# Optimization experiments

Hardware: AMD Instinct MI355X
Metric: run time of the kernel (lower is better)

The kernel has to match this reference:

```python
import jax, jax.numpy as jnp
import numpy as np

D = 1024; NHEAD = 8; NQ = 256; B = 8; HM = 64; WM = 64; S = HM * WM; FF = 4 * D
EPS_LN = 1e-5


def _ln(x, g, b):
    m = x.mean(-1, keepdims=True)
    v = ((x - m) ** 2).mean(-1, keepdims=True)
    return (x - m) / jnp.sqrt(v + EPS_LN) * g + b


def _self_attn(x, w_in, b_in, w_out, b_out, nhead):
    # x: [L, B, D] (torch MultiheadAttention, batch_first=False, eval mode)
    L, Bn, Dm = x.shape
    hd = Dm // nhead
    qkv = x @ w_in.T + b_in  # [L, B, 3D]
    q, k, v = jnp.split(qkv, 3, axis=-1)
    sp = lambda t: t.reshape(L, Bn, nhead, hd).transpose(1, 2, 0, 3)  # [B, H, L, hd]
    q, k, v = sp(q), sp(k), sp(v)
    attn = jax.nn.softmax(jnp.einsum('bhqd,bhkd->bhqk', q, k) / float(hd) ** 0.5, axis=-1)
    out = jnp.einsum('bhqk,bhkd->bhqd', attn, v)
    out = out.transpose(2, 0, 1, 3).reshape(L, Bn, Dm)
    return out @ w_out.T + b_out


def setup_inputs() -> dict:
    key = jax.random.key(0)
    ks = iter(jax.random.split(key, 40))
    nrm = lambda shape: jax.random.normal(next(ks), shape, jnp.float32) * 0.02
    return dict(
        query=jax.random.normal(next(ks), (NQ, B, D), jnp.float32),
        memory=jax.random.normal(next(ks), (S, B, D), jnp.float32),
        prev_mask=jax.random.uniform(next(ks), (B, NQ, HM, WM), dtype=jnp.float32),
        h_mem=HM, w_mem=WM,
        sa_in_w=nrm((3 * D, D)), sa_in_b=jnp.zeros((3 * D,), jnp.float32),
        sa_out_w=nrm((D, D)), sa_out_b=jnp.zeros((D,), jnp.float32),
        ln1_g=jnp.ones((D,), jnp.float32), ln1_b=jnp.zeros((D,), jnp.float32),
        ln2_g=jnp.ones((D,), jnp.float32), ln2_b=jnp.zeros((D,), jnp.float32),
        ln3_g=jnp.ones((D,), jnp.float32), ln3_b=jnp.zeros((D,), jnp.float32),
        wq=nrm((D, D)), bq=jnp.zeros((D,), jnp.float32),
        wk=nrm((D, D)), bk=jnp.zeros((D,), jnp.float32),
        wv=nrm((D, D)), bv=jnp.zeros((D,), jnp.float32),
        wo=nrm((D, D)), bo=jnp.zeros((D,), jnp.float32),
        w1=nrm((FF, D)), b1=jnp.zeros((FF,), jnp.float32),
        w2=nrm((D, FF)), b2=jnp.zeros((D,), jnp.float32),
        mask_w=nrm((S, D)), mask_b=jnp.zeros((S,), jnp.float32),
    )


def reference(query, memory, prev_mask, h_mem, w_mem,
              sa_in_w, sa_in_b, sa_out_w, sa_out_b,
              ln1_g, ln1_b, ln2_g, ln2_b, ln3_g, ln3_b,
              wq, bq, wk, bk, wv, bv, wo, bo,
              w1, b1, w2, b2, mask_w, mask_b):
    nq, Bn, d_model = query.shape
    # --- self attention block ---
    q_norm = _ln(query, ln1_g, ln1_b)
    q2 = _self_attn(q_norm, sa_in_w, sa_in_b, sa_out_w, sa_out_b, NHEAD)
    query = query + q2
    # --- masked cross attention (single-head, as in source) ---
    Q = (_ln(query, ln2_g, ln2_b) @ wq.T + bq).transpose(1, 0, 2)  # [B, NQ, D]
    K = (memory @ wk.T + bk).transpose(1, 0, 2)                    # [B, S, D]
    V = (memory @ wv.T + bv).transpose(1, 0, 2)                    # [B, S, D]
    scores = jnp.einsum('bqd,bsd->bqs', Q, K) / float(d_model) ** 0.5
    scores = scores + jnp.log(prev_mask.reshape(Bn, nq, -1) + 1e-6)
    attn = jax.nn.softmax(scores, axis=-1)
    attn_out = jnp.einsum('bqs,bsd->bqd', attn, V).transpose(1, 0, 2)  # [NQ, B, D]
    query = query + (attn_out @ wo.T + bo)
    # --- FFN ---
    h = jax.nn.gelu(_ln(query, ln3_g, ln3_b) @ w1.T + b1, approximate=False)
    query = query + (h @ w2.T + b2)
    # --- mask prediction ---
    q_for_mask = query.transpose(1, 0, 2)                # [B, NQ, D]
    mask_logits = q_for_mask @ mask_w.T + mask_b          # [B, NQ, H*W]
    pred_mask = jax.nn.sigmoid(mask_logits.reshape(Bn, nq, h_mem, w_mem))
    return (query, pred_mask)
```

## Files before the change

### kernel.cpp

```cpp
#include <hip/hip_runtime.h>
#include <cstdint>


typedef __attribute__((ext_vector_type(8))) __bf16 bf16x8;
typedef __attribute__((ext_vector_type(4))) float f32x4;
typedef __attribute__((ext_vector_type(8))) unsigned short ushort8;
typedef __attribute__((ext_vector_type(4))) unsigned short ushort4v;

__device__ __forceinline__ unsigned short f2bf(float f) {
  return __builtin_bit_cast(unsigned short, (__bf16)f);
}

__global__ __launch_bounds__(256) void cast_bf16_kernel(const float* __restrict__ in,
                                                        unsigned short* __restrict__ out,
                                                        int n8) {
  int i = blockIdx.x * 256 + threadIdx.x;
  if (i >= n8) return;
  const float4* p = (const float4*)in + (size_t)i * 2;
  float4 a = p[0], b = p[1];
  ushort8 o;
  o[0] = f2bf(a.x); o[1] = f2bf(a.y); o[2] = f2bf(a.z); o[3] = f2bf(a.w);
  o[4] = f2bf(b.x); o[5] = f2bf(b.y); o[6] = f2bf(b.z); o[7] = f2bf(b.w);
  ((ushort8*)out)[i] = o;
}

struct CastSegs {
  const float* src[9];
  int cum[10];
};
__global__ __launch_bounds__(256) void cast_multi_kernel(CastSegs cs,
                                                         unsigned short* __restrict__ out) {
  int i = blockIdx.x * 256 + threadIdx.x;
  if (i >= cs.cum[9]) return;
  int s = 0;
  while (i >= cs.cum[s + 1]) s++;
  const float4* p = (const float4*)cs.src[s] + (size_t)(i - cs.cum[s]) * 2;
  float4 a = p[0], b = p[1];
  ushort8 o;
  o[0] = f2bf(a.x); o[1] = f2bf(a.y); o[2] = f2bf(a.z); o[3] = f2bf(a.w);
  o[4] = f2bf(b.x); o[5] = f2bf(b.y); o[6] = f2bf(b.z); o[7] = f2bf(b.w);
  ((ushort8*)out)[i] = o;
}

__global__ __launch_bounds__(256) void bias_concat_kernel(const float* __restrict__ a,
                                                          const float* __restrict__ b,
                                                          float* __restrict__ o) {
  int i = blockIdx.x * 256 + threadIdx.x;
  o[i] = i < 1024 ? a[i] : b[i - 1024];
}

__global__ __launch_bounds__(256) void ln_bf16_kernel(const float* __restrict__ x,
                                                      const float* __restrict__ g,
                                                      const float* __restrict__ b,
                                                      unsigned short* __restrict__ out) {
  int row = blockIdx.x, tid = threadIdx.x;
  const float4* xr = (const float4*)(x + (size_t)row * 1024);
  float4 v = xr[tid];
  float s = v.x + v.y + v.z + v.w;
  float sq = v.x * v.x + v.y * v.y + v.z * v.z + v.w * v.w;
#pragma unroll
  for (int o = 32; o > 0; o >>= 1) { s += __shfl_xor(s, o); sq += __shfl_xor(sq, o); }
  __shared__ float red[8];
  int wave = tid >> 6, lane = tid & 63;
  if (lane == 0) { red[wave] = s; red[4 + wave] = sq; }
  __syncthreads();
  float ts = red[0] + red[1] + red[2] + red[3];
  float tq = red[4] + red[5] + red[6] + red[7];
  float mean = ts * (1.f / 1024.f);
  float var = tq * (1.f / 1024.f) - mean * mean;
  float rstd = rsqrtf(var + 1e-5f);
  float4 gv = ((const float4*)g)[tid];
  float4 bv = ((const float4*)b)[tid];
  ushort4v o;
  o[0] = f2bf((v.x - mean) * rstd * gv.x + bv.x);
  o[1] = f2bf((v.y - mean) * rstd * gv.y + bv.y);
  o[2] = f2bf((v.z - mean) * rstd * gv.z + bv.z);
  o[3] = f2bf((v.w - mean) * rstd * gv.w + bv.w);
  ((ushort4v*)(out + (size_t)row * 1024))[tid] = o;
}

template <bool MASK, int CNT>
__global__ __launch_bounds__(256) void softmax_bf16_kernel(const float* __restrict__ sc,
                                                           const float* __restrict__ pm,
                                                           unsigned short* __restrict__ out,
                                                           float scale) {
  const int L = CNT * 256;
  int row = blockIdx.x, tid = threadIdx.x;
  const float* sr = sc + (size_t)row * L;
  float vals[CNT];
  float mx = -1e30f;
#pragma unroll
  for (int i = 0; i < CNT; i++) {
    int idx = tid + (i << 8);
    float v = sr[idx] * scale;
    if (MASK) v += __logf(pm[(size_t)row * L + idx] + 1e-6f);
    vals[i] = v;
    mx = fmaxf(mx, v);
  }
#pragma unroll
  for (int o = 32; o > 0; o >>= 1) mx = fmaxf(mx, __shfl_xor(mx, o));
  __shared__ float red[8];
  int wave = tid >> 6, lane = tid & 63;
  if (lane == 0) red[wave] = mx;
  __syncthreads();
  mx = fmaxf(fmaxf(red[0], red[1]), fmaxf(red[2], red[3]));
  float sum = 0.f;
#pragma unroll
  for (int i = 0; i < CNT; i++) { vals[i] = __expf(vals[i] - mx); sum += vals[i]; }
#pragma unroll
  for (int o = 32; o > 0; o >>= 1) sum += __shfl_xor(sum, o);
  if (lane == 0) red[4 + wave] = sum;
  __syncthreads();
  float rs = 1.f / (red[4] + red[5] + red[6] + red[7]);
#pragma unroll
  for (int i = 0; i < CNT; i++)
    out[(size_t)row * L + tid + (i << 8)] = f2bf(vals[i] * rs);
}

__global__ __launch_bounds__(256) void transpose_bf16_kernel(
    const unsigned short* __restrict__ in, unsigned short* __restrict__ out,
    long in_off, int in_rs, long in_hi, long in_lo, int zdiv,
    long out_off, int out_rs, long out_hi, long out_lo) {
  __shared__ unsigned short t[32][33];
  int z = blockIdx.z;
  int zh = z / zdiv, zl = z % zdiv;
  const unsigned short* ib = in + in_off + (long)zh * in_hi + (long)zl * in_lo;
  unsigned short* ob = out + out_off + (long)zh * out_hi + (long)zl * out_lo;
  int i0 = blockIdx.x * 32;
  int j0 = blockIdx.y * 32;
  int tx = threadIdx.x & 31, ty = threadIdx.x >> 5;
#pragma unroll
  for (int r = ty; r < 32; r += 8) t[r][tx] = ib[(long)(j0 + r) * in_rs + i0 + tx];
  __syncthreads();
#pragma unroll
  for (int r = ty; r < 32; r += 8) ob[(long)(i0 + r) * out_rs + j0 + tx] = t[tx][r];
}

template <int TM, bool AF32, bool BIAS, int ACT, bool RES, bool OUTF, bool OUTB, bool KVSPLIT>
__global__ __launch_bounds__(256) void gemm_nt_kernel(
    const void* __restrict__ Av, long a_off, int lda, long a_hi, long a_lo,
    const unsigned short* __restrict__ B, long b_off, int ldb, long b_hi, long b_lo,
    const float* __restrict__ bias, const float* __restrict__ Res,
    float* __restrict__ Cf, long c_off, int ldc, long c_hi, long c_lo,
    unsigned short* __restrict__ Cb, long cb_off, int ldcb, long cb_hi, long cb_lo,
    int K, int zdiv) {
  constexpr int MI = TM / 32;
  __shared__ unsigned short As[2 * TM * 32];
  __shared__ unsigned short Bs[2 * 128 * 32];
  int tid = threadIdx.x;
  int wave = tid >> 6, lane = tid & 63;
  int z = blockIdx.z, zh = z / zdiv, zl = z % zdiv;
  long m0 = (long)blockIdx.x * TM, n0 = (long)blockIdx.y * 128;

  const unsigned short* Bb = B + b_off + zh * b_hi + zl * b_lo + n0 * ldb;
  const unsigned short* Ab16 = nullptr;
  const float* Abf = nullptr;
  if constexpr (AF32)
    Abf = (const float*)Av + a_off + zh * a_hi + zl * a_lo + m0 * lda;
  else
    Ab16 = (const unsigned short*)Av + a_off + zh * a_hi + zl * a_lo + m0 * lda;

  int srow = lane >> 2;
  int scol = (lane & 3) * 8;
  int wm = (wave >> 1) * (TM / 2), wn = (wave & 1) * 64;
  int fr = lane & 15;
  int ko = (lane >> 4) * 8;

  f32x4 acc[MI][4] = {};

  auto stage = [&](int buf, int k0) {
    unsigned short* Ad = As + buf * (TM * 32);
    unsigned short* Bd = Bs + buf * (128 * 32);
    if constexpr (AF32) {
      int row = tid >> 1;
      int cs = (tid & 1) * 16;
      const float* ap = Abf + (long)row * lda + k0 + cs;
      float4 f0 = ((const float4*)ap)[0];
      float4 f1 = ((const float4*)ap)[1];
      float4 f2 = ((const float4*)ap)[2];
      float4 f3 = ((const float4*)ap)[3];
      ushort8 u0, u1;
      u0[0] = f2bf(f0.x); u0[1] = f2bf(f0.y); u0[2] = f2bf(f0.z); u0[3] = f2bf(f0.w);
      u0[4] = f2bf(f1.x); u0[5] = f2bf(f1.y); u0[6] = f2bf(f1.z); u0[7] = f2bf(f1.w);
      u1[0] = f2bf(f2.x); u1[1] = f2bf(f2.y); u1[2] = f2bf(f2.z); u1[3] = f2bf(f2.w);
      u1[4] = f2bf(f3.x); u1[5] = f2bf(f3.y); u1[6] = f2bf(f3.z); u1[7] = f2bf(f3.w);
      ushort8* dst = (ushort8*)(Ad + row * 32 + cs);
      dst[0] = u0;
      dst[1] = u1;
    } else {
#pragma unroll
      for (int is = 0; is < TM / 64; is++) {
        int rbase = wave * (TM / 4) + is * 16;
        const unsigned short* g = Ab16 + (long)(rbase + srow) * lda + k0 + scol;
        __builtin_amdgcn_global_load_lds(
            (const __attribute__((address_space(1))) unsigned int*)g,
            (__attribute__((address_space(3))) unsigned int*)(Ad + rbase * 32), 16, 0, 0);
      }
    }
#pragma unroll
    for (int is = 0; is < 2; is++) {
      int rbase = wave * 32 + is * 16;
      const unsigned short* g = Bb + (long)(rbase + srow) * ldb + k0 + scol;
      __builtin_amdgcn_global_load_lds(
          (const __attribute__((address_space(1))) unsigned int*)g,
          (__attribute__((address_space(3))) unsigned int*)(Bd + rbase * 32), 16, 0, 0);
    }
  };

  stage(0, 0);
  int cur = 0;
  for (int k0 = 0; k0 < K; k0 += 32, cur ^= 1) {
    __syncthreads();
    if (k0 + 32 < K) stage(cur ^ 1, k0 + 32);

    const unsigned short* Ar = As + cur * (TM * 32);
    const unsigned short* Br = Bs + cur * (128 * 32);
    bf16x8 af[MI], bfv[4];
#pragma unroll
    for (int i = 0; i < MI; i++)
      af[i] = *(const bf16x8*)(Ar + (wm + i * 16 + fr) * 32 + ko);
#pragma unroll
    for (int j = 0; j < 4; j++)
      bfv[j] = *(const bf16x8*)(Br + (wn + j * 16 + fr) * 32 + ko);
#pragma unroll
    for (int i = 0; i < MI; i++)
#pragma unroll
      for (int j = 0; j < 4; j++)
        acc[i][j] = __builtin_amdgcn_mfma_f32_16x16x32_bf16(af[i], bfv[j], acc[i][j], 0, 0, 0);
  }

  long cfo = c_off + zh * c_hi + zl * c_lo;
  long cbo = cb_off + zh * cb_hi + zl * cb_lo;
  int rq = (lane >> 4) * 4;
#pragma unroll
  for (int i = 0; i < MI; i++) {
    long rbase = m0 + wm + i * 16 + rq;
#pragma unroll
    for (int j = 0; j < 4; j++) {
      long cc = n0 + wn + j * 16 + fr;
      float bsv = BIAS ? bias[cc] : 0.f;
      long p = KVSPLIT ? ((cc >> 10) * cb_hi + (cc & 1023)) : cc;
#pragma unroll
      for (int r = 0; r < 4; r++) {
        float v = acc[i][j][r] + bsv;
        long ro = rbase + r;
        if constexpr (RES) v += Res[cfo + ro * ldc + cc];
        if constexpr (ACT == 1) v = 0.5f * v * (1.f + erff(v * 0.7071067811865475f));
        if constexpr (ACT == 2) v = 1.f / (1.f + __expf(-v));
        if constexpr (OUTF) Cf[cfo + ro * ldc + cc] = v;
        if constexpr (OUTB) Cb[cbo + ro * ldcb + p] = f2bf(v);
      }
    }
  }
}

__global__ __launch_bounds__(512, 2) void gemm256_kv_kernel(
    const unsigned short* __restrict__ A,
    const unsigned short* __restrict__ B,
    const float* __restrict__ bias,
    unsigned short* __restrict__ C,
    long plane) {
  __shared__ __align__(1024) unsigned short lds[4][2][8192];
  const int K = 1024, NT = 32;
  int tid = threadIdx.x;
  int wave = tid >> 6, lane = tid & 63;
  int wr = wave >> 2, wc = wave & 3;
  int fr = lane & 15, hi = lane >> 4;

  int l = blockIdx.x >> 3;
  long m0 = (long)((blockIdx.x & 7) * 16 + (l >> 3)) * 256;
  int n0 = (l & 7) * 256;

  const unsigned short* Ab = A + m0 * K;
  const unsigned short* Bb = B + (long)n0 * K;

  int lr = lane >> 2;
  int lc = (((lane & 3) ^ ((lane >> 5) << 1)) << 3);

  auto stageA = [&](int buf, int k0) {
    const unsigned short* g0 = Ab + (long)(wave * 16 + lr) * K + k0 + lc;
    __builtin_amdgcn_global_load_lds(
        (const __attribute__((address_space(1))) unsigned int*)g0,
        (__attribute__((address_space(3))) unsigned int*)&lds[buf][0][wave * 512], 16, 0, 0);
    const unsigned short* g1 = g0 + (long)128 * K;
    __builtin_amdgcn_global_load_lds(
        (const __attribute__((address_space(1))) unsigned int*)g1,
        (__attribute__((address_space(3))) unsigned int*)&lds[buf][0][4096 + wave * 512], 16, 0, 0);
  };
  auto stageB = [&](int buf, int k0) {
    const unsigned short* g0 = Bb + (long)(wave * 16 + lr) * K + k0 + lc;
    __builtin_amdgcn_global_load_lds(
        (const __attribute__((address_space(1))) unsigned int*)g0,
        (__attribute__((address_space(3))) unsigned int*)&lds[buf][1][wave * 512], 16, 0, 0);
    const unsigned short* g1 = g0 + (long)128 * K;
    __builtin_amdgcn_global_load_lds(
        (const __attribute__((address_space(1))) unsigned int*)g1,
        (__attribute__((address_space(3))) unsigned int*)&lds[buf][1][4096 + wave * 512], 16, 0, 0);
  };

  int cbel = ((hi * 16) ^ ((fr >> 3) << 5)) >> 1;
  int aoff = (wr * 128 + fr) * 32 + cbel;
  int boff = (wc * 64 + fr) * 32 + cbel;

  f32x4 acc[8][4] = {};

#pragma unroll
  for (int t = 0; t < 3; t++) { stageA(t, t * 32); stageB(t, t * 32); }
  asm volatile("s_waitcnt vmcnt(8)" ::: "memory");
  __builtin_amdgcn_s_barrier();

#pragma unroll 4
  for (int t = 0; t < NT; t++) {
    int buf = t & 3;
    const unsigned short* Abuf = &lds[buf][0][0];
    const unsigned short* Bbuf = &lds[buf][1][0];
    bf16x8 af[4], bfv[4];

#pragma unroll
    for (int i = 0; i < 4; i++)
      af[i] = *(const bf16x8*)(Abuf + aoff + i * 512);
#pragma unroll
    for (int n = 0; n < 4; n++)
      bfv[n] = *(const bf16x8*)(Bbuf + boff + n * 512);
    if (t + 3 < NT) stageA((t + 3) & 3, (t + 3) * 32);
    __builtin_amdgcn_s_barrier();
    asm volatile("s_waitcnt lgkmcnt(0)" ::: "memory");
    __builtin_amdgcn_sched_barrier(0);
    __builtin_amdgcn_s_setprio(1);
#pragma unroll
    for (int i = 0; i < 4; i++)
#pragma unroll
      for (int n = 0; n < 4; n++)
        acc[i][n] = __builtin_amdgcn_mfma_f32_16x16x32_bf16(af[i], bfv[n], acc[i][n], 0, 0, 0);
    __builtin_amdgcn_s_setprio(0);
    __builtin_amdgcn_s_barrier();

#pragma unroll
    for (int i = 0; i < 4; i++)
      af[i] = *(const bf16x8*)(Abuf + aoff + 2048 + i * 512);
    if (t + 3 < NT) stageB((t + 3) & 3, (t + 3) * 32);
    __builtin_amdgcn_s_barrier();
    asm volatile("s_waitcnt lgkmcnt(0)" ::: "memory");
    __builtin_amdgcn_sched_barrier(0);
    __builtin_amdgcn_s_setprio(1);
#pragma unroll
    for (int i = 0; i < 4; i++)
#pragma unroll
      for (int n = 0; n < 4; n++)
        acc[4 + i][n] = __builtin_amdgcn_mfma_f32_16x16x32_bf16(af[i], bfv[n], acc[4 + i][n], 0, 0, 0);
    __builtin_amdgcn_s_setprio(0);
    asm volatile("s_waitcnt vmcnt(8)" ::: "memory");
    __builtin_amdgcn_s_barrier();
  }

  int rq = hi * 4;
#pragma unroll
  for (int i = 0; i < 8; i++) {
    long r0 = m0 + wr * 128 + i * 16 + rq;
#pragma unroll
    for (int n = 0; n < 4; n++) {
      int cc = n0 + wc * 64 + n * 16 + fr;
      float bsv = bias[cc];
      long p = (long)(cc >> 10) * plane + (cc & 1023);
#pragma unroll
      for (int r = 0; r < 4; r++)
        C[p + (r0 + r) * 1024] = f2bf(acc[i][n][r] + bsv);
    }
  }
}

template <int TM, bool AF32, bool BIAS, int ACT, bool RES, bool OUTF, bool OUTB, bool KVSPLIT = false>
static void launch_gemm(hipStream_t s, int M, int N, int K, int nz, int zdiv,
                        const void* A, long a_off, int lda, long a_hi, long a_lo,
                        const unsigned short* B, long b_off, int ldb, long b_hi, long b_lo,
                        const float* bias, const float* Res,
                        float* Cf, long c_off, int ldc, long c_hi, long c_lo,
                        unsigned short* Cb, long cb_off, int ldcb, long cb_hi, long cb_lo) {
  dim3 g(M / TM, N / 128, nz);
  gemm_nt_kernel<TM, AF32, BIAS, ACT, RES, OUTF, OUTB, KVSPLIT><<<g, dim3(256), 0, s>>>(
      A, a_off, lda, a_hi, a_lo, B, b_off, ldb, b_hi, b_lo, bias, Res,
      Cf, c_off, ldc, c_hi, c_lo, Cb, cb_off, ldcb, cb_hi, cb_lo, K, zdiv);
}

static const long WB_SAIN = 0;
static const long WB_SAOUT = 6291456;
static const long WB_WQ = 8388608;
static const long WB_WK = 10485760;
static const long WB_WV = 12582912;
static const long WB_WO = 14680064;
static const long WB_W1 = 16777216;
static const long WB_W2 = 25165824;
static const long WB_MW = 33554432;
static const long OF_K = 41943040;
static const long OF_V = 109051904;
static const long OF_QKV = 176160768;
static const long OF_BKV = 187695104;
static const long OF_SC = 188743680;
static const long OF_P = 222298112;
static const long OF_QN = 239075328;
static const long OF_Q = 243269632;
static const long OF_CTX = 247463936;
static const long OF_MEMBF = 251658240;
static const size_t FAST_WS = 318767104;

extern "C" void kernel_launch(void* const* d_in, const int* in_sizes, int n_in,
                              void* d_out, int out_size, void* d_ws, size_t ws_size,
                              hipStream_t stream) {
  (void)in_sizes; (void)n_in; (void)out_size;
  const float* query = (const float*)d_in[0];
  const float* memoryp = (const float*)d_in[1];
  const float* prev_mask = (const float*)d_in[2];
  const float* sa_in_w = (const float*)d_in[5];
  const float* sa_in_b = (const float*)d_in[6];
  const float* sa_out_w = (const float*)d_in[7];
  const float* sa_out_b = (const float*)d_in[8];
  const float* ln1_g = (const float*)d_in[9], * ln1_b = (const float*)d_in[10];
  const float* ln2_g = (const float*)d_in[11], * ln2_b = (const float*)d_in[12];
  const float* ln3_g = (const float*)d_in[13], * ln3_b = (const float*)d_in[14];
  const float* wq = (const float*)d_in[15], * bq = (const float*)d_in[16];
  const float* wk = (const float*)d_in[17], * bk = (const float*)d_in[18];
  const float* wv = (const float*)d_in[19], * bv = (const float*)d_in[20];
  const float* wo = (const float*)d_in[21], * bo = (const float*)d_in[22];
  const float* w1 = (const float*)d_in[23], * b1 = (const float*)d_in[24];
  const float* w2 = (const float*)d_in[25], * b2 = (const float*)d_in[26];
  const float* mask_w = (const float*)d_in[27], * mask_b = (const float*)d_in[28];

  uint8_t* ws = (uint8_t*)d_ws;
  auto bf = [&](long off) { return (unsigned short*)(ws + off); };
  auto fp = [&](long off) { return (float*)(ws + off); };
  unsigned short* ZB = nullptr;
  float* ZF = nullptr;
  const bool fast = ws_size >= FAST_WS;

  {
    CastSegs cs;
    const float* srcs[9] = {sa_in_w, sa_out_w, wq, wk, wv, wo, w1, w2, mask_w};
    int n8s[9] = {393216, 131072, 131072, 131072, 131072, 131072, 524288, 524288, 524288};
    int c = 0;
    for (int i = 0; i < 9; i++) { cs.src[i] = srcs[i]; cs.cum[i] = c; c += n8s[i]; }
    cs.cum[9] = c;
    cast_multi_kernel<<<dim3((c + 255) / 256), dim3(256), 0, stream>>>(cs, bf(0));
  }

  ln_bf16_kernel<<<2048, 256, 0, stream>>>(query, ln1_g, ln1_b, bf(OF_QN));

  launch_gemm<128, false, true, 0, false, false, true>(stream, 2048, 3072, 1024, 1, 1,
      bf(OF_QN), 0, 1024, 0, 0, bf(WB_SAIN), 0, 1024, 0, 0, sa_in_b, nullptr,
      ZF, 0, 0, 0, 0, bf(OF_QKV), 0, 3072, 0, 0);

  launch_gemm<128, false, false, 0, false, true, false>(stream, 256, 256, 128, 64, 8,
      bf(OF_QKV), 0, 24576, 3072, 128,
      bf(OF_QKV), 1024, 24576, 3072, 128, nullptr, nullptr,
      fp(OF_SC), 0, 256, 524288, 65536, ZB, 0, 0, 0, 0);

  softmax_bf16_kernel<false, 1><<<16384, 256, 0, stream>>>(
      fp(OF_SC), nullptr, bf(OF_P), 0.08838834764831845f);

  transpose_bf16_kernel<<<dim3(4, 8, 64), 256, 0, stream>>>(
      bf(OF_QKV), bf(OF_QN), 2048L, 24576, 3072L, 128L, 8, 0L, 256, 262144L, 32768L);

  launch_gemm<64, false, false, 0, false, false, true>(stream, 256, 128, 256, 64, 8,
      bf(OF_P), 0, 256, 524288, 65536,
      bf(OF_QN), 0, 256, 262144, 32768, nullptr, nullptr,
      ZF, 0, 0, 0, 0, bf(OF_CTX), 0, 8192, 1024, 128);

  launch_gemm<64, false, true, 0, true, true, false>(stream, 2048, 1024, 1024, 1, 1,
      bf(OF_CTX), 0, 1024, 0, 0, bf(WB_SAOUT), 0, 1024, 0, 0, sa_out_b, query,
      fp(OF_QKV), 0, 1024, 0, 0, ZB, 0, 0, 0, 0);

  ln_bf16_kernel<<<2048, 256, 0, stream>>>(fp(OF_QKV), ln2_g, ln2_b, bf(OF_QN));

  launch_gemm<64, false, true, 0, false, false, true>(stream, 2048, 1024, 1024, 1, 1,
      bf(OF_QN), 0, 1024, 0, 0, bf(WB_WQ), 0, 1024, 0, 0, bq, nullptr,
      ZF, 0, 0, 0, 0, bf(OF_Q), 0, 1024, 0, 0);

  bias_concat_kernel<<<8, 256, 0, stream>>>(bk, bv, fp(OF_BKV));
  if (fast) {
    cast_bf16_kernel<<<16384, 256, 0, stream>>>(memoryp, bf(OF_MEMBF), 4194304);
    gemm256_kv_kernel<<<dim3(1024), dim3(512), 0, stream>>>(
        bf(OF_MEMBF), bf(WB_WK), fp(OF_BKV), bf(OF_K), 33554432L);
  } else {
    launch_gemm<128, true, true, 0, false, false, true, true>(stream, 32768, 2048, 1024, 1, 1,
        memoryp, 0, 1024, 0, 0, bf(WB_WK), 0, 1024, 0, 0, fp(OF_BKV), nullptr,
        ZF, 0, 0, 0, 0, bf(OF_K), 0, 1024, 33554432, 0);
  }

  launch_gemm<128, false, false, 0, false, true, false>(stream, 256, 4096, 1024, 8, 1,
      bf(OF_Q), 0, 8192, 1024, 0,
      bf(OF_K), 0, 8192, 1024, 0, nullptr, nullptr,
      fp(OF_SC), 0, 4096, 1048576, 0, ZB, 0, 0, 0, 0);

  softmax_bf16_kernel<true, 16><<<2048, 256, 0, stream>>>(
      fp(OF_SC), prev_mask, bf(OF_P), 0.03125f);

  transpose_bf16_kernel<<<dim3(32, 128, 8), 256, 0, stream>>>(
      bf(OF_V), bf(OF_K), 0L, 8192, 1024L, 0L, 1, 0L, 4096, 4194304L, 0L);

  launch_gemm<64, false, false, 0, false, false, true>(stream, 256, 1024, 4096, 8, 1,
      bf(OF_P), 0, 4096, 1048576, 0,
      bf(OF_K), 0, 4096, 4194304, 0, nullptr, nullptr,
      ZF, 0, 0, 0, 0, bf(OF_CTX), 0, 8192, 1024, 0);

  launch_gemm<64, false, true, 0, true, true, false>(stream, 2048, 1024, 1024, 1, 1,
      bf(OF_CTX), 0, 1024, 0, 0, bf(WB_WO), 0, 1024, 0, 0, bo, fp(OF_QKV),
      fp(OF_SC), 0, 1024, 0, 0, ZB, 0, 0, 0, 0);

  ln_bf16_kernel<<<2048, 256, 0, stream>>>(fp(OF_SC), ln3_g, ln3_b, bf(OF_QN));

  launch_gemm<128, false, true, 1, false, false, true>(stream, 2048, 4096, 1024, 1, 1,
      bf(OF_QN), 0, 1024, 0, 0, bf(WB_W1), 0, 1024, 0, 0, b1, nullptr,
      ZF, 0, 0, 0, 0, bf(OF_P), 0, 4096, 0, 0);

  launch_gemm<64, false, true, 0, true, true, true>(stream, 2048, 1024, 4096, 1, 1,
      bf(OF_P), 0, 4096, 0, 0, bf(WB_W2), 0, 4096, 0, 0, b2, fp(OF_SC),
      (float*)d_out, 0, 1024, 0, 0, bf(OF_CTX), 0, 1024, 0, 0);

  launch_gemm<128, false, true, 2, false, true, false>(stream, 256, 4096, 1024, 8, 1,
      bf(OF_CTX), 0, 8192, 1024, 0,
      bf(WB_MW), 0, 1024, 0, 0, mask_b, nullptr,
      (float*)d_out + 2097152, 0, 4096, 1048576, 0, ZB, 0, 0, 0, 0);
}
```

Before: 949.2 us.

## Software-pipeline LDS fragment loads across K tiles in KV GEMM

Restructures the KV projection GEMM main loop so the next tile's A/B fragments are loaded from LDS while the current tile's MFMAs run, using ping-pong register sets and partial lgkmcnt waits instead of full drains. It also drops one barrier per half-step and peels the tail iterations with tuned vmcnt counts. The launch bound no longer requests two blocks per CU, letting the compiler use more registers for the extra fragment buffers at the risk of lower occupancy.

```diff
diff --git a/kernel.cpp b/kernel.cpp
--- a/kernel.cpp
+++ b/kernel.cpp
@@ -254,7 +254,45 @@
   }
 }
 
-__global__ __launch_bounds__(512, 2) void gemm256_kv_kernel(
+#define KV_TILE(T, AFA, BFV, AFAN, BFVN, VM1, LG2, DOSTAGE, DONEXT)            \
+  {                                                                            \
+    const unsigned short* Abuf = &lds[(T) & 3][0][0];                          \
+    const unsigned short* AbufN = &lds[((T) + 1) & 3][0][0];                   \
+    const unsigned short* BbufN = &lds[((T) + 1) & 3][1][0];                   \
+    _Pragma("unroll") for (int i = 0; i < 4; i++)                              \
+        afB[i] = *(const bf16x8*)(Abuf + aoff + 2048 + i * 512);               \
+    if (DOSTAGE) stageA(((T) + 3) & 3, ((T) + 3) * 32);                        \
+    __builtin_amdgcn_sched_barrier(0);                                         \
+    asm volatile("s_waitcnt lgkmcnt(4)" ::: "memory");                         \
+    __builtin_amdgcn_sched_barrier(0);                                         \
+    __builtin_amdgcn_s_setprio(1);                                             \
+    _Pragma("unroll") for (int i = 0; i < 4; i++)                              \
+        _Pragma("unroll") for (int n = 0; n < 4; n++)                          \
+            acc[i][n] = __builtin_amdgcn_mfma_f32_16x16x32_bf16(               \
+                AFA[i], BFV[n], acc[i][n], 0, 0, 0);                           \
+    __builtin_amdgcn_s_setprio(0);                                             \
+    asm volatile("s_waitcnt vmcnt(" #VM1 ")" ::: "memory");                    \
+    __builtin_amdgcn_s_barrier();                                              \
+    if (DONEXT) {                                                              \
+      _Pragma("unroll") for (int i = 0; i < 4; i++)                            \
+          AFAN[i] = *(const bf16x8*)(AbufN + aoff + i * 512);                  \
+      _Pragma("unroll") for (int n = 0; n < 4; n++)                            \
+          BFVN[n] = *(const bf16x8*)(BbufN + boff + n * 512);                  \
+    }                                                                          \
+    if (DOSTAGE) stageB(((T) + 3) & 3, ((T) + 3) * 32);                        \
+    __builtin_amdgcn_sched_barrier(0);                                         \
+    asm volatile("s_waitcnt lgkmcnt(" #LG2 ")" ::: "memory");                  \
+    __builtin_amdgcn_sched_barrier(0);                                         \
+    __builtin_amdgcn_s_setprio(1);                                             \
+    _Pragma("unroll") for (int i = 0; i < 4; i++)                              \
+        _Pragma("unroll") for (int n = 0; n < 4; n++)                          \
+            acc[4 + i][n] = __builtin_amdgcn_mfma_f32_16x16x32_bf16(           \
+                afB[i], BFV[n], acc[4 + i][n], 0, 0, 0);                       \
+    __builtin_amdgcn_s_setprio(0);                                             \
+    __builtin_amdgcn_s_barrier();                                              \
+  }
+
+__global__ __launch_bounds__(512) void gemm256_kv_kernel(
     const unsigned short* __restrict__ A,
     const unsigned short* __restrict__ B,
     const float* __restrict__ bias,
@@ -303,55 +341,29 @@
   int boff = (wc * 64 + fr) * 32 + cbel;
 
   f32x4 acc[8][4] = {};
+  bf16x8 afA_p[4], bfv_p[4], afA_q[4], bfv_q[4], afB[4];
 
 #pragma unroll
   for (int t = 0; t < 3; t++) { stageA(t, t * 32); stageB(t, t * 32); }
   asm volatile("s_waitcnt vmcnt(8)" ::: "memory");
   __builtin_amdgcn_s_barrier();
-
-#pragma unroll 4
-  for (int t = 0; t < NT; t++) {
-    int buf = t & 3;
-    const unsigned short* Abuf = &lds[buf][0][0];
-    const unsigned short* Bbuf = &lds[buf][1][0];
-    bf16x8 af[4], bfv[4];
-
-#pragma unroll
-    for (int i = 0; i < 4; i++)
-      af[i] = *(const bf16x8*)(Abuf + aoff + i * 512);
-#pragma unroll
-    for (int n = 0; n < 4; n++)
-      bfv[n] = *(const bf16x8*)(Bbuf + boff + n * 512);
-    if (t + 3 < NT) stageA((t + 3) & 3, (t + 3) * 32);
-    __builtin_amdgcn_s_barrier();
-    asm volatile("s_waitcnt lgkmcnt(0)" ::: "memory");
-    __builtin_amdgcn_sched_barrier(0);
-    __builtin_amdgcn_s_setprio(1);
-#pragma unroll
-    for (int i = 0; i < 4; i++)
-#pragma unroll
-      for (int n = 0; n < 4; n++)
-        acc[i][n] = __builtin_amdgcn_mfma_f32_16x16x32_bf16(af[i], bfv[n], acc[i][n], 0, 0, 0);
-    __builtin_amdgcn_s_setprio(0);
-    __builtin_amdgcn_s_barrier();
-
-#pragma unroll
-    for (int i = 0; i < 4; i++)
-      af[i] = *(const bf16x8*)(Abuf + aoff + 2048 + i * 512);
-    if (t + 3 < NT) stageB((t + 3) & 3, (t + 3) * 32);
-    __builtin_amdgcn_s_barrier();
-    asm volatile("s_waitcnt lgkmcnt(0)" ::: "memory");
-    __builtin_amdgcn_sched_barrier(0);
-    __builtin_amdgcn_s_setprio(1);
-#pragma unroll
-    for (int i = 0; i < 4; i++)
-#pragma unroll
-      for (int n = 0; n < 4; n++)
-        acc[4 + i][n] = __builtin_amdgcn_mfma_f32_16x16x32_bf16(af[i], bfv[n], acc[4 + i][n], 0, 0, 0);
-    __builtin_amdgcn_s_setprio(0);
-    asm volatile("s_waitcnt vmcnt(8)" ::: "memory");
-    __builtin_amdgcn_s_barrier();
-  }
+  {
+    const unsigned short* Abuf0 = &lds[0][0][0];
+    const unsigned short* Bbuf0 = &lds[0][1][0];
+#pragma unroll
+    for (int i = 0; i < 4; i++) afA_p[i] = *(const bf16x8*)(Abuf0 + aoff + i * 512);
+#pragma unroll
+    for (int n = 0; n < 4; n++) bfv_p[n] = *(const bf16x8*)(Bbuf0 + boff + n * 512);
+  }
+
+  for (int t = 0; t < 28; t += 2) {
+    KV_TILE(t, afA_p, bfv_p, afA_q, bfv_q, 6, 8, 1, 1)
+    KV_TILE(t + 1, afA_q, bfv_q, afA_p, bfv_p, 6, 8, 1, 1)
+  }
+  KV_TILE(28, afA_p, bfv_p, afA_q, bfv_q, 6, 8, 1, 1)
+  KV_TILE(29, afA_q, bfv_q, afA_p, bfv_p, 4, 8, 0, 1)
+  KV_TILE(30, afA_p, bfv_p, afA_q, bfv_q, 0, 8, 0, 1)
+  KV_TILE(31, afA_q, bfv_q, afA_p, bfv_p, 0, 0, 0, 0)
 
   int rq = hi * 4;
 #pragma unroll
```

After: 944.0 us. About the same (-0.6%).
